# Optimization experiments

Measured on AMD Instinct MI355X. Metric: run time of the kernel, lower is better.

The kernel has to match this reference:

```python
import jax, jax.numpy as jnp
import numpy as np

B, H, N, F = 64, 24, 32, 256

def setup_inputs() -> dict:
    key = jax.random.key(0)
    ks = jax.random.split(key, 6)
    s = 1.0 / np.sqrt(F)
    return {
        "Q": jax.random.normal(ks[0], (B, N, F), jnp.float32),
        "K": jax.random.normal(ks[1], (B, H, N, F), jnp.float32),
        "V": jax.random.normal(ks[2], (B, H, N, F), jnp.float32),
        "Wq": jax.random.normal(ks[3], (N, F, F), jnp.float32) * s,
        "bq": jnp.zeros((N, F), jnp.float32),
        "Wk": jax.random.normal(ks[4], (N, H, F, F), jnp.float32) * s,
        "bk": jnp.zeros((N, H, F), jnp.float32),
        "Wv": jax.random.normal(ks[5], (N, H, F, F), jnp.float32) * s,
        "bv": jnp.zeros((N, H, F), jnp.float32),
    }

def reference(Q, K, V, Wq, bq, Wk, bk, Wv, bv):
    # Per-node query projection: [B,N,F]
    QWq = jnp.einsum('bnf,nfg->bng', Q, Wq) + bq
    # Per-node, per-encoder-step key/value projections: [B,N,H,F]
    KWk = jnp.einsum('bhnf,nhfg->bnhg', K, Wk) + bk
    VWv = jnp.einsum('bhnf,nhfg->bnhg', V, Wv) + bv
    # Attention scores over the H encoder steps (no sqrt(F) scaling, as in source)
    logits = jnp.einsum('bng,bnhg->bnh', QWq, KWk)
    scores = jax.nn.softmax(logits, axis=-1)          # [B,N,H]
    heads = jnp.einsum('bnh,bnhg->bng', scores, VWv)  # [B,N,F]
    return heads, scores
```

## Files before the change

kernel.cpp:

```cpp
#include <hip/hip_runtime.h>

typedef __attribute__((ext_vector_type(8))) short short8;
typedef __attribute__((ext_vector_type(4))) float f32x4;

#define B_ 64
#define H_ 24
#define N_ 32
#define F_ 256

__device__ __forceinline__ float bf2f(unsigned short u) {
    return __uint_as_float(((unsigned)u) << 16);
}
__device__ __forceinline__ unsigned short f2bf(float f) {
    unsigned u = __float_as_uint(f);
    u += 0x7fffu + ((u >> 16) & 1u);
    return (unsigned short)(u >> 16);
}
__device__ __forceinline__ unsigned pack_hi(float f0, float f1) {
    return (__float_as_uint(f0) >> 16) | (__float_as_uint(f1) & 0xffff0000u);
}
__device__ __forceinline__ float res_lo(float f) {
    return f - __uint_as_float(__float_as_uint(f) & 0xffff0000u);
}

union U4S8 { uint4 u; short8 s; };

template<bool SPLIT>
__device__ __forceinline__ void gemm_direct(
    const float* __restrict__ Ab, long rstride,
    const float* __restrict__ Wb, int wv, int lane,
    f32x4 acc[4][4])
{
    const int l15  = lane & 15;
    const int quad = lane >> 4;
    const float* abase = Ab + (long)l15 * rstride + quad * 8;
    const float* wbase = Wb + (quad * 8) * F_ + wv * 64 + l15;

    #pragma unroll
    for (int ks = 0; ks < 8; ks++) {
        const int k0 = ks * 32;
        short8 ah[4], al[4];
        #pragma unroll
        for (int mi = 0; mi < 4; mi++) {
            const float* ap = abase + (long)(mi * 16) * rstride + k0;
            float4 a0 = *(const float4*)ap;
            float4 a1 = *(const float4*)(ap + 4);
            U4S8 h;
            h.u.x = pack_hi(a0.x, a0.y); h.u.y = pack_hi(a0.z, a0.w);
            h.u.z = pack_hi(a1.x, a1.y); h.u.w = pack_hi(a1.z, a1.w);
            ah[mi] = h.s;
            if (SPLIT) {
                U4S8 l;
                l.u.x = pack_hi(res_lo(a0.x), res_lo(a0.y));
                l.u.y = pack_hi(res_lo(a0.z), res_lo(a0.w));
                l.u.z = pack_hi(res_lo(a1.x), res_lo(a1.y));
                l.u.w = pack_hi(res_lo(a1.z), res_lo(a1.w));
                al[mi] = l.s;
            }
        }
        #pragma unroll
        for (int ni = 0; ni < 4; ni++) {
            const float* wp = wbase + (long)k0 * F_ + ni * 16;
            float w[8];
            #pragma unroll
            for (int j = 0; j < 8; j++) w[j] = wp[j * F_];
            U4S8 bh;
            bh.u.x = pack_hi(w[0], w[1]); bh.u.y = pack_hi(w[2], w[3]);
            bh.u.z = pack_hi(w[4], w[5]); bh.u.w = pack_hi(w[6], w[7]);
            if (SPLIT) {
                U4S8 bl;
                bl.u.x = pack_hi(res_lo(w[0]), res_lo(w[1]));
                bl.u.y = pack_hi(res_lo(w[2]), res_lo(w[3]));
                bl.u.z = pack_hi(res_lo(w[4]), res_lo(w[5]));
                bl.u.w = pack_hi(res_lo(w[6]), res_lo(w[7]));
                #pragma unroll
                for (int mi = 0; mi < 4; mi++) {
                    acc[mi][ni] = __builtin_amdgcn_mfma_f32_16x16x32_bf16(al[mi], bh.s, acc[mi][ni], 0, 0, 0);
                    acc[mi][ni] = __builtin_amdgcn_mfma_f32_16x16x32_bf16(ah[mi], bl.s, acc[mi][ni], 0, 0, 0);
                    acc[mi][ni] = __builtin_amdgcn_mfma_f32_16x16x32_bf16(ah[mi], bh.s, acc[mi][ni], 0, 0, 0);
                }
            } else {
                #pragma unroll
                for (int mi = 0; mi < 4; mi++)
                    acc[mi][ni] = __builtin_amdgcn_mfma_f32_16x16x32_bf16(ah[mi], bh.s, acc[mi][ni], 0, 0, 0);
            }
        }
    }
}

__global__ __launch_bounds__(64) void k_qproj(
    const float* __restrict__ Q, const float* __restrict__ Wq,
    const float* __restrict__ bq, float* __restrict__ qws)
{
    const int n  = blockIdx.x;
    const int wv = blockIdx.y;
    const int lane = threadIdx.x;
    f32x4 acc[4][4];
    #pragma unroll
    for (int i = 0; i < 4; i++)
        #pragma unroll
        for (int j = 0; j < 4; j++) acc[i][j] = (f32x4){0.f, 0.f, 0.f, 0.f};

    gemm_direct<true>(Q + n * F_, (long)(N_ * F_), Wq + (long)n * F_ * F_,
                      wv, lane, acc);

    const int l15 = lane & 15, quad = lane >> 4;
    const float* bias = bq + n * F_;
    float* dst = qws + (long)n * (B_ * F_);
    #pragma unroll
    for (int ni = 0; ni < 4; ni++) {
        int g = wv * 64 + ni * 16 + l15;
        float bb = bias[g];
        #pragma unroll
        for (int mi = 0; mi < 4; mi++)
            #pragma unroll
            for (int reg = 0; reg < 4; reg++) {
                int r = mi * 16 + quad * 4 + reg;
                dst[r * 256 + g] = acc[mi][ni][reg] + bb;
            }
    }
}

__global__ __launch_bounds__(256) void k_kvproj(
    const float* __restrict__ Kx, const float* __restrict__ Vx,
    const float* __restrict__ Wk, const float* __restrict__ bk,
    const float* __restrict__ Wv, const float* __restrict__ bv,
    const float* __restrict__ qws, float* __restrict__ logits,
    unsigned short* __restrict__ vws)
{
    const int nh = blockIdx.x;
    const int n = nh / H_;
    const int h = nh - n * H_;
    const bool isV = (blockIdx.y != 0);
    const float* X    = isV ? Vx : Kx;
    const float* W    = (isV ? Wv : Wk) + (long)nh * F_ * F_;
    const float* bias = (isV ? bv : bk) + nh * F_;

    __shared__ unsigned short outT[64 * 256];
    __shared__ float slog[64];
    const int t = threadIdx.x;
    if (!isV && t < 64) slog[t] = 0.f;

    f32x4 acc[4][4];
    #pragma unroll
    for (int i = 0; i < 4; i++)
        #pragma unroll
        for (int j = 0; j < 4; j++) acc[i][j] = (f32x4){0.f, 0.f, 0.f, 0.f};

    const float* Xb = X + (long)(h * N_ + n) * F_;
    if (isV) gemm_direct<false>(Xb, (long)(H_ * N_ * F_), W, t >> 6, t & 63, acc);
    else     gemm_direct<true >(Xb, (long)(H_ * N_ * F_), W, t >> 6, t & 63, acc);

    const int lane = t & 63, wv = t >> 6, l15 = lane & 15, quad = lane >> 4;

    if (!isV) {
        __syncthreads();
        const float* qrow = qws + (long)n * (B_ * F_);
        #pragma unroll
        for (int mi = 0; mi < 4; mi++) {
            float p[4] = {0.f, 0.f, 0.f, 0.f};
            #pragma unroll
            for (int ni = 0; ni < 4; ni++) {
                int g = wv * 64 + ni * 16 + l15;
                float bb = bias[g];
                #pragma unroll
                for (int reg = 0; reg < 4; reg++) {
                    int r = mi * 16 + quad * 4 + reg;
                    p[reg] += (acc[mi][ni][reg] + bb) * qrow[r * 256 + g];
                }
            }
            #pragma unroll
            for (int off = 1; off < 16; off <<= 1)
                #pragma unroll
                for (int reg = 0; reg < 4; reg++)
                    p[reg] += __shfl_xor(p[reg], off, 64);
            if (l15 == 0)
                #pragma unroll
                for (int reg = 0; reg < 4; reg++)
                    atomicAdd(&slog[mi * 16 + quad * 4 + reg], p[reg]);
        }
        __syncthreads();
        if (t < 64) logits[(long)nh * 64 + t] = slog[t];
    } else {
        #pragma unroll
        for (int ni = 0; ni < 4; ni++) {
            int g = wv * 64 + ni * 16 + l15;
            float bb = bias[g];
            #pragma unroll
            for (int mi = 0; mi < 4; mi++)
                #pragma unroll
                for (int reg = 0; reg < 4; reg++) {
                    int r = mi * 16 + quad * 4 + reg;
                    outT[r * 256 + g] = f2bf(acc[mi][ni][reg] + bb);
                }
        }
        __syncthreads();
        unsigned short* dst = vws + (long)nh * (B_ * F_);
        #pragma unroll
        for (int it = 0; it < 8; it++) {
            int row = it * 8 + (t >> 5);
            int c = t & 31;
            uint4 v = *(const uint4*)(&outT[row * 256 + c * 8]);
            *(uint4*)(dst + row * 256 + c * 8) = v;
        }
    }
}

__global__ __launch_bounds__(64) void k_attn(
    const float* __restrict__ logits,
    const unsigned short* __restrict__ vws,
    float* __restrict__ out)
{
    const int bx = blockIdx.x;
    const int b = bx >> 5;
    const int n = bx & 31;
    const int t = threadIdx.x;
    __shared__ float sl[24], se[24];
    if (t < 24) sl[t] = logits[(long)(n * H_ + t) * 64 + b];
    __syncthreads();
    float mx = -1e30f;
    #pragma unroll
    for (int h = 0; h < H_; h++) mx = fmaxf(mx, sl[h]);
    if (t < 24) se[t] = expf(sl[t] - mx);
    __syncthreads();
    float den = 0.f;
    #pragma unroll
    for (int h = 0; h < H_; h++) den += se[h];
    float inv = 1.0f / den;
    if (t < 24)
        out[(long)B_ * N_ * F_ + (long)(b * N_ + n) * H_ + t] = se[t] * inv;

    const int g0 = t * 4;
    float hv[4] = {0.f, 0.f, 0.f, 0.f};
    #pragma unroll
    for (int h = 0; h < H_; h++) {
        float s = se[h] * inv;
        const unsigned short* vp = vws + (((long)(n * H_ + h) * 64 + b) << 8) + g0;
        union { uint2 u; unsigned short e[4]; } vv;
        vv.u = *(const uint2*)vp;
        #pragma unroll
        for (int j = 0; j < 4; j++) hv[j] += s * bf2f(vv.e[j]);
    }
    float4 ov = make_float4(hv[0], hv[1], hv[2], hv[3]);
    *(float4*)(out + ((long)b * N_ + n) * F_ + g0) = ov;
}

extern "C" void kernel_launch(void* const* d_in, const int* in_sizes, int n_in,
                              void* d_out, int out_size, void* d_ws, size_t ws_size,
                              hipStream_t stream) {
    const float* Q  = (const float*)d_in[0];
    const float* K  = (const float*)d_in[1];
    const float* V  = (const float*)d_in[2];
    const float* Wq = (const float*)d_in[3];
    const float* bq = (const float*)d_in[4];
    const float* Wk = (const float*)d_in[5];
    const float* bk = (const float*)d_in[6];
    const float* Wv = (const float*)d_in[7];
    const float* bv = (const float*)d_in[8];

    char* ws = (char*)d_ws;
    float* qws          = (float*)ws;
    float* logits       = (float*)(ws + 2097152);
    unsigned short* vws = (unsigned short*)(ws + 2097152 + 262144);

    k_qproj<<<dim3(N_, 4), 64, 0, stream>>>(Q, Wq, bq, qws);
    k_kvproj<<<dim3(N_ * H_, 2), 256, 0, stream>>>(K, V, Wk, bk, Wv, bv, qws, logits, vws);
    k_attn<<<B_ * N_, 64, 0, stream>>>(logits, vws, (float*)d_out);
}
```

Baseline: 521.8 us.

## Stage GEMM operands through double-buffered LDS with async global-to-LDS loads

Replaces direct per-lane global loads in the projection GEMMs with a double-buffered LDS pipeline. Each stage is filled with global_load_lds 16-byte copies, so the next K-slice loads while the current one is computed, and the W reads become coalesced. The staging buffers share a union with the epilogue scratch, and the Q projection moves to one 256-thread block per node instead of four single-wave blocks. This adds barriers per K-step and about 80KB of LDS per block, which may limit occupancy, and it relies on hand-written vmcnt waits.

```diff
diff --git a/kernel.cpp b/kernel.cpp
--- a/kernel.cpp
+++ b/kernel.cpp
@@ -25,24 +25,75 @@
 
 union U4S8 { uint4 u; short8 s; };
 
+__device__ __forceinline__ void gload16(const float* g, float* l) {
+    __builtin_amdgcn_global_load_lds(
+        (const __attribute__((address_space(1))) void*)g,
+        (__attribute__((address_space(3))) void*)l, 16, 0, 0);
+}
+
+struct StageBufs {
+    float A[2][64 * 32];
+    float W[2][32 * 256];
+};
+union Smem {
+    StageBufs s;
+    unsigned short outT[64 * 256];
+    float slog[64];
+};
+
 template<bool SPLIT>
-__device__ __forceinline__ void gemm_direct(
+__device__ __forceinline__ void gemm_f32(
     const float* __restrict__ Ab, long rstride,
-    const float* __restrict__ Wb, int wv, int lane,
-    f32x4 acc[4][4])
+    const float* __restrict__ Wb, Smem& sm, f32x4 acc[4][4])
 {
+    const int t    = threadIdx.x;
+    const int lane = t & 63;
+    const int wv   = t >> 6;
     const int l15  = lane & 15;
     const int quad = lane >> 4;
-    const float* abase = Ab + (long)l15 * rstride + quad * 8;
-    const float* wbase = Wb + (quad * 8) * F_ + wv * 64 + l15;
-
+
+    const int aseg0 = wv * 2;
+    const int arow0 = aseg0 * 8 + (lane >> 3);
+    const int acol  = (lane & 7) * 4;
+
+    auto STAGE = [&](int ks, int b) {
+        const int k0 = ks * 32;
+        #pragma unroll
+        for (int i = 0; i < 2; i++) {
+            const float* src = Ab + (long)(arow0 + i * 8) * rstride + k0 + acol;
+            gload16(src, &sm.s.A[b][(aseg0 + i) * 256]);
+        }
+        #pragma unroll
+        for (int j = 0; j < 8; j++) {
+            const int k = wv * 8 + j;
+            const float* src = Wb + (long)(k0 + k) * 256 + lane * 4;
+            gload16(src, &sm.s.W[b][k * 256]);
+        }
+    };
+
+    STAGE(0, 0);
     #pragma unroll
     for (int ks = 0; ks < 8; ks++) {
-        const int k0 = ks * 32;
+        const int cur = ks & 1;
+        asm volatile("s_waitcnt lgkmcnt(0)" ::: "memory");
+        __builtin_amdgcn_s_barrier();
+        asm volatile("" ::: "memory");
+        if (ks < 7) {
+            STAGE(ks + 1, cur ^ 1);
+            asm volatile("s_waitcnt vmcnt(10)" ::: "memory");
+        } else {
+            asm volatile("s_waitcnt vmcnt(0)" ::: "memory");
+        }
+        __builtin_amdgcn_s_barrier();
+        asm volatile("" ::: "memory");
+
+        const float* Af = sm.s.A[cur];
+        const float* Wf = sm.s.W[cur];
+
         short8 ah[4], al[4];
         #pragma unroll
         for (int mi = 0; mi < 4; mi++) {
-            const float* ap = abase + (long)(mi * 16) * rstride + k0;
+            const float* ap = Af + (mi * 16 + l15) * 32 + quad * 8;
             float4 a0 = *(const float4*)ap;
             float4 a1 = *(const float4*)(ap + 4);
             U4S8 h;
@@ -60,10 +111,10 @@
         }
         #pragma unroll
         for (int ni = 0; ni < 4; ni++) {
-            const float* wp = wbase + (long)k0 * F_ + ni * 16;
+            const int g = wv * 64 + ni * 16 + l15;
             float w[8];
             #pragma unroll
-            for (int j = 0; j < 8; j++) w[j] = wp[j * F_];
+            for (int j = 0; j < 8; j++) w[j] = Wf[(quad * 8 + j) * 256 + g];
             U4S8 bh;
             bh.u.x = pack_hi(w[0], w[1]); bh.u.y = pack_hi(w[2], w[3]);
             bh.u.z = pack_hi(w[4], w[5]); bh.u.w = pack_hi(w[6], w[7]);
@@ -88,22 +139,21 @@
     }
 }
 
-__global__ __launch_bounds__(64) void k_qproj(
+__global__ __launch_bounds__(256, 2) void k_qproj(
     const float* __restrict__ Q, const float* __restrict__ Wq,
     const float* __restrict__ bq, float* __restrict__ qws)
 {
-    const int n  = blockIdx.x;
-    const int wv = blockIdx.y;
-    const int lane = threadIdx.x;
+    const int n = blockIdx.x;
+    __shared__ Smem sm;
     f32x4 acc[4][4];
     #pragma unroll
     for (int i = 0; i < 4; i++)
         #pragma unroll
         for (int j = 0; j < 4; j++) acc[i][j] = (f32x4){0.f, 0.f, 0.f, 0.f};
 
-    gemm_direct<true>(Q + n * F_, (long)(N_ * F_), Wq + (long)n * F_ * F_,
-                      wv, lane, acc);
-
+    gemm_f32<true>(Q + n * F_, (long)(N_ * F_), Wq + (long)n * F_ * F_, sm, acc);
+
+    const int t = threadIdx.x, lane = t & 63, wv = t >> 6;
     const int l15 = lane & 15, quad = lane >> 4;
     const float* bias = bq + n * F_;
     float* dst = qws + (long)n * (B_ * F_);
@@ -121,7 +171,7 @@
     }
 }
 
-__global__ __launch_bounds__(256) void k_kvproj(
+__global__ __launch_bounds__(256, 2) void k_kvproj(
     const float* __restrict__ Kx, const float* __restrict__ Vx,
     const float* __restrict__ Wk, const float* __restrict__ bk,
     const float* __restrict__ Wv, const float* __restrict__ bv,
@@ -136,10 +186,8 @@
     const float* W    = (isV ? Wv : Wk) + (long)nh * F_ * F_;
     const float* bias = (isV ? bv : bk) + nh * F_;
 
-    __shared__ unsigned short outT[64 * 256];
-    __shared__ float slog[64];
+    __shared__ Smem sm;
     const int t = threadIdx.x;
-    if (!isV && t < 64) slog[t] = 0.f;
 
     f32x4 acc[4][4];
     #pragma unroll
@@ -148,12 +196,14 @@
         for (int j = 0; j < 4; j++) acc[i][j] = (f32x4){0.f, 0.f, 0.f, 0.f};
 
     const float* Xb = X + (long)(h * N_ + n) * F_;
-    if (isV) gemm_direct<false>(Xb, (long)(H_ * N_ * F_), W, t >> 6, t & 63, acc);
-    else     gemm_direct<true >(Xb, (long)(H_ * N_ * F_), W, t >> 6, t & 63, acc);
+    if (isV) gemm_f32<false>(Xb, (long)(H_ * N_ * F_), W, sm, acc);
+    else     gemm_f32<true >(Xb, (long)(H_ * N_ * F_), W, sm, acc);
 
     const int lane = t & 63, wv = t >> 6, l15 = lane & 15, quad = lane >> 4;
 
     if (!isV) {
+        __syncthreads();
+        if (t < 64) sm.slog[t] = 0.f;
         __syncthreads();
         const float* qrow = qws + (long)n * (B_ * F_);
         #pragma unroll
@@ -177,11 +227,12 @@
             if (l15 == 0)
                 #pragma unroll
                 for (int reg = 0; reg < 4; reg++)
-                    atomicAdd(&slog[mi * 16 + quad * 4 + reg], p[reg]);
-        }
-        __syncthreads();
-        if (t < 64) logits[(long)nh * 64 + t] = slog[t];
+                    atomicAdd(&sm.slog[mi * 16 + quad * 4 + reg], p[reg]);
+        }
+        __syncthreads();
+        if (t < 64) logits[(long)nh * 64 + t] = sm.slog[t];
     } else {
+        __syncthreads();
         #pragma unroll
         for (int ni = 0; ni < 4; ni++) {
             int g = wv * 64 + ni * 16 + l15;
@@ -191,7 +242,7 @@
                 #pragma unroll
                 for (int reg = 0; reg < 4; reg++) {
                     int r = mi * 16 + quad * 4 + reg;
-                    outT[r * 256 + g] = f2bf(acc[mi][ni][reg] + bb);
+                    sm.outT[r * 256 + g] = f2bf(acc[mi][ni][reg] + bb);
                 }
         }
         __syncthreads();
@@ -200,7 +251,7 @@
         for (int it = 0; it < 8; it++) {
             int row = it * 8 + (t >> 5);
             int c = t & 31;
-            uint4 v = *(const uint4*)(&outT[row * 256 + c * 8]);
+            uint4 v = *(const uint4*)(&sm.outT[row * 256 + c * 8]);
             *(uint4*)(dst + row * 256 + c * 8) = v;
         }
     }
@@ -263,7 +314,7 @@
     float* logits       = (float*)(ws + 2097152);
     unsigned short* vws = (unsigned short*)(ws + 2097152 + 262144);
 
-    k_qproj<<<dim3(N_, 4), 64, 0, stream>>>(Q, Wq, bq, qws);
+    k_qproj<<<N_, 256, 0, stream>>>(Q, Wq, bq, qws);
     k_kvproj<<<dim3(N_ * H_, 2), 256, 0, stream>>>(K, V, Wk, bk, Wv, bv, qws, logits, vws);
     k_attn<<<B_ * N_, 64, 0, stream>>>(logits, vws, (float*)d_out);
 }
```

Result: faster. 486.7 us (-6.7%).
